# Performance work log

Measured on AMD Instinct MI355X. Metric: run time of the kernel, lower is better.

Reference implementation:

```python
import jax, jax.numpy as jnp
import numpy as np

EMBED_DIM = 128
FFN_DIM = 512
N_NODES = 50000
N_EDGES = 800000
LN_EPS = 1e-5


def setup_inputs() -> dict:
    key = jax.random.key(0)
    ks = jax.random.split(key, 8)
    s = 1.0 / np.sqrt(EMBED_DIM)
    return {
        "x": jax.random.normal(ks[0], (N_NODES, EMBED_DIM), jnp.float32),
        "edge_indices": jax.random.randint(ks[1], (2, N_EDGES), 0, N_NODES, dtype=jnp.int32),
        "W_qkv": jax.random.normal(ks[2], (EMBED_DIM, 3 * EMBED_DIM), jnp.float32) * s,
        "b_qkv": jnp.zeros((3 * EMBED_DIM,), jnp.float32),
        "W1": jax.random.normal(ks[3], (EMBED_DIM, FFN_DIM), jnp.float32) * s,
        "b1": jnp.zeros((FFN_DIM,), jnp.float32),
        "W2": jax.random.normal(ks[4], (FFN_DIM, EMBED_DIM), jnp.float32) * (1.0 / np.sqrt(FFN_DIM)),
        "b2": jnp.zeros((EMBED_DIM,), jnp.float32),
        "g1": jnp.ones((EMBED_DIM,), jnp.float32),
        "be1": jnp.zeros((EMBED_DIM,), jnp.float32),
        "g2": jnp.ones((EMBED_DIM,), jnp.float32),
        "be2": jnp.zeros((EMBED_DIM,), jnp.float32),
    }


def _layernorm(x, g, b):
    mu = jnp.mean(x, axis=-1, keepdims=True)
    var = jnp.mean(jnp.square(x - mu), axis=-1, keepdims=True)
    return (x - mu) * jax.lax.rsqrt(var + LN_EPS) * g + b


def _self_attention(x, edge_indices, W_qkv, b_qkv):
    n = x.shape[0]
    scale = x.shape[1] ** (-0.5)
    qkv = x @ W_qkv + b_qkv
    q, k, v = jnp.split(qkv, 3, axis=1)
    src, dst = edge_indices[0], edge_indices[1]  # row (softmax segment), col
    # per-edge logits: [E]
    alpha = jnp.sum(q[src] * k[dst], axis=1) * scale
    # segment (per-row) stable softmax
    m = jax.ops.segment_max(alpha, src, num_segments=n)
    e = jnp.exp(alpha - m[src])
    denom = jax.ops.segment_sum(e, src, num_segments=n)
    w = e / denom[src]  # [E]
    # sparse.mm: out[i] = sum_{(i,j) in E} w_ij * v[j]
    return jax.ops.segment_sum(w[:, None] * v[dst], src, num_segments=n)


def reference(x, edge_indices, W_qkv, b_qkv, W1, b1, W2, b2, g1, be1, g2, be2):
    # norm_first = False (post-norm), dropout = 0
    x = _layernorm(x + _self_attention(x, edge_indices, W_qkv, b_qkv), g1, be1)
    h = jax.nn.relu(x @ W1 + b1) @ W2 + b2
    x = _layernorm(x + h, g2, be2)
    return x
```

## Files before the change

### kernel.cpp

```cpp
#include <hip/hip_runtime.h>
#include <math.h>

#define NN 50000
#define NE 800000
#define ED 128
#define FD 512
#define QKV_BLOCKS (NN / 16)
#define HIST_BLOCKS ((NE / 4 + 255) / 256)
#define SCAN_BLOCKS ((NN + 255) / 256)

typedef __attribute__((ext_vector_type(8))) short bf16x8;
typedef __attribute__((ext_vector_type(4))) float f32x4;

static __device__ __forceinline__ float wave_sum(float x) {
#pragma unroll
  for (int off = 32; off > 0; off >>= 1) x += __shfl_xor(x, off, 64);
  return x;
}

static __device__ __forceinline__ int wave_sum_i(int x) {
#pragma unroll
  for (int off = 32; off > 0; off >>= 1) x += __shfl_xor(x, off, 64);
  return x;
}

static __device__ __forceinline__ unsigned short f2bf(float f) {
  union { float f; unsigned u; } c; c.f = f;
  unsigned r = c.u + 0x7fffu + ((c.u >> 16) & 1u);
  return (unsigned short)(r >> 16);
}

static __device__ __forceinline__ float2 bfpair(unsigned u) {
  union { unsigned a; float f; } lo, hi;
  lo.a = u << 16; hi.a = u & 0xffff0000u;
  return make_float2(lo.f, hi.f);
}

__global__ void k_prep(const float* __restrict__ Wqkv, const float* __restrict__ W1,
                       const float* __restrict__ W2, unsigned short* __restrict__ WqkvF,
                       unsigned short* __restrict__ W1F, unsigned short* __restrict__ W2F,
                       int* __restrict__ deg) {
  int idx = blockIdx.x * 256 + threadIdx.x;
  if (idx < NN) deg[idx] = 0;
  if (idx < 49152) {
    int j = idx & 7, l = (idx >> 3) & 63, kb = (idx >> 9) & 3, t = idx >> 11;
    int k = kb * 32 + (l >> 4) * 8 + j, n = t * 16 + (l & 15);
    WqkvF[idx] = f2bf(Wqkv[k * 384 + n]);
  }
  {
    int j = idx & 7, l = (idx >> 3) & 63, kb = (idx >> 9) & 3, t = idx >> 11;
    int k = kb * 32 + (l >> 4) * 8 + j, n = t * 16 + (l & 15);
    W1F[idx] = f2bf(W1[k * 512 + n]);
  }
  {
    int j = idx & 7, l = (idx >> 3) & 63, kb = (idx >> 9) & 15, t = idx >> 13;
    int k = kb * 32 + (l >> 4) * 8 + j, n = t * 16 + (l & 15);
    W2F[idx] = f2bf(W2[k * 128 + n]);
  }
}

__global__ __launch_bounds__(256) void k_qkv_hist(
    const float* __restrict__ X, const unsigned short* __restrict__ WqkvF,
    const float* __restrict__ B, unsigned short* __restrict__ q,
    unsigned short* __restrict__ k, unsigned short* __restrict__ v,
    const int* __restrict__ src, int* __restrict__ deg) {
  __shared__ unsigned short xs[16][136];
  const int tid = threadIdx.x;
  if (blockIdx.x >= QKV_BLOCKS) {
    const int e0 = ((blockIdx.x - QKV_BLOCKS) * 256 + tid) * 4;
    if (e0 < NE) {
      int4 s4 = *(const int4*)&src[e0];
      atomicAdd(&deg[s4.x], 1);
      atomicAdd(&deg[s4.y], 1);
      atomicAdd(&deg[s4.z], 1);
      atomicAdd(&deg[s4.w], 1);
    }
    return;
  }
  const int row0 = blockIdx.x * 16;
  for (int idx = tid; idx < 512; idx += 256) {
    int r = idx >> 5, c4 = (idx & 31) << 2;
    float4 val = *(const float4*)&X[(size_t)(row0 + r) * ED + c4];
    xs[r][c4] = f2bf(val.x); xs[r][c4 + 1] = f2bf(val.y);
    xs[r][c4 + 2] = f2bf(val.z); xs[r][c4 + 3] = f2bf(val.w);
  }
  __syncthreads();
  const int wv = tid >> 6, lane = tid & 63;
  const int ln = lane & 15, quad = lane >> 4;
  const int koff = quad * 8;
  bf16x8 a[4];
#pragma unroll
  for (int kb = 0; kb < 4; kb++) a[kb] = *(const bf16x8*)&xs[ln][kb * 32 + koff];
  for (int g = 0; g < 3; g++) {
    const int t0 = wv * 6 + g * 2;
    bf16x8 b[2][4];
#pragma unroll
    for (int j = 0; j < 2; j++)
#pragma unroll
      for (int kb = 0; kb < 4; kb++)
        b[j][kb] = *(const bf16x8*)&WqkvF[(size_t)(((t0 + j) * 4 + kb) * 64 + lane) * 8];
    f32x4 acc[2];
#pragma unroll
    for (int j = 0; j < 2; j++) acc[j] = (f32x4){0.f, 0.f, 0.f, 0.f};
#pragma unroll
    for (int kb = 0; kb < 4; kb++)
#pragma unroll
      for (int j = 0; j < 2; j++)
        acc[j] = __builtin_amdgcn_mfma_f32_16x16x32_bf16(a[kb], b[j][kb], acc[j], 0, 0, 0);
#pragma unroll
    for (int j = 0; j < 2; j++) {
      const int col = (t0 + j) * 16 + ln;
      const float bias = B[col];
      unsigned short* dst = (col < 128) ? q : (col < 256) ? k : v;
      const int c = col & 127;
#pragma unroll
      for (int r = 0; r < 4; r++)
        dst[(size_t)(row0 + quad * 4 + r) * ED + c] = f2bf(acc[j][r] + bias);
    }
  }
}

__global__ __launch_bounds__(256) void k_scan1(const int* __restrict__ deg,
                                               int* __restrict__ blocksum) {
  const int tid = threadIdx.x;
  const int i = blockIdx.x * 256 + tid;
  int d = (i < NN) ? deg[i] : 0;
  int w = wave_sum_i(d);
  __shared__ int ws[4];
  if ((tid & 63) == 0) ws[tid >> 6] = w;
  __syncthreads();
  if (tid == 0) blocksum[blockIdx.x] = ws[0] + ws[1] + ws[2] + ws[3];
}

__global__ __launch_bounds__(256) void k_scan3(const int* __restrict__ deg,
                                               const int* __restrict__ blocksum,
                                               int* __restrict__ row_start,
                                               int* __restrict__ cursor) {
  __shared__ int bs[256];
  __shared__ int s[256];
  const int t = threadIdx.x;
  int bsv = (t < SCAN_BLOCKS) ? blocksum[t] : 0;
  bs[t] = bsv;
  __syncthreads();
  for (int off = 1; off < 256; off <<= 1) {
    int add = (t >= off) ? bs[t - off] : 0;
    __syncthreads();
    bs[t] += add;
    __syncthreads();
  }
  const int blockpre = (blockIdx.x > 0) ? bs[blockIdx.x - 1] : 0;
  const int i = blockIdx.x * 256 + t;
  int d = (i < NN) ? deg[i] : 0;
  s[t] = d;
  __syncthreads();
  for (int off = 1; off < 256; off <<= 1) {
    int add = (t >= off) ? s[t - off] : 0;
    __syncthreads();
    s[t] += add;
    __syncthreads();
  }
  const int pre = blockpre + s[t] - d;
  if (i < NN) {
    row_start[i] = pre;
    cursor[i] = pre;
  }
  if (i == NN) row_start[NN] = pre;
}

__global__ void k_scatter(const int* __restrict__ src, const int* __restrict__ dst,
                          int* __restrict__ cursor, int* __restrict__ colidx) {
  const int e0 = (blockIdx.x * 256 + threadIdx.x) * 4;
  if (e0 < NE) {
    int4 s4 = *(const int4*)&src[e0];
    int4 d4 = *(const int4*)&dst[e0];
    colidx[atomicAdd(&cursor[s4.x], 1)] = d4.x;
    colidx[atomicAdd(&cursor[s4.y], 1)] = d4.y;
    colidx[atomicAdd(&cursor[s4.z], 1)] = d4.z;
    colidx[atomicAdd(&cursor[s4.w], 1)] = d4.w;
  }
}

template <bool FULL>
static __device__ __forceinline__ void attn_chunk(
    int base, int cnt, int grp, int gl, int lane, const float* qf,
    const unsigned short* __restrict__ k, const unsigned short* __restrict__ v,
    const int* __restrict__ colidx, float& l, float* ax) {
  const int C = FULL ? 16 : cnt;
  int colreg = 0;
  if (lane < C) colreg = colidx[base + lane];
#pragma unroll
  for (int it = 0; it < 4; it++) {
    const int t = it * 4 + grp;
    const bool act = FULL || t < C;
    const int srcl = act ? t : 0;
    const int c = __shfl(colreg, srcl, 64);
    uint4 kw = *(const uint4*)&k[(size_t)c * ED + gl * 8];
    uint4 vw = *(const uint4*)&v[(size_t)c * ED + gl * 8];
    float2 k0 = bfpair(kw.x), k1 = bfpair(kw.y), k2 = bfpair(kw.z), k3 = bfpair(kw.w);
    float dot = qf[0] * k0.x + qf[1] * k0.y + qf[2] * k1.x + qf[3] * k1.y +
                qf[4] * k2.x + qf[5] * k2.y + qf[6] * k3.x + qf[7] * k3.y;
    dot += __shfl_xor(dot, 1, 64);
    dot += __shfl_xor(dot, 2, 64);
    dot += __shfl_xor(dot, 4, 64);
    dot += __shfl_xor(dot, 8, 64);
    const float e = act ? __expf(dot * 0.08838834764831845f) : 0.f;
    l += e;
    float2 v0 = bfpair(vw.x), v1 = bfpair(vw.y), v2 = bfpair(vw.z), v3 = bfpair(vw.w);
    ax[0] = fmaf(e, v0.x, ax[0]); ax[1] = fmaf(e, v0.y, ax[1]);
    ax[2] = fmaf(e, v1.x, ax[2]); ax[3] = fmaf(e, v1.y, ax[3]);
    ax[4] = fmaf(e, v2.x, ax[4]); ax[5] = fmaf(e, v2.y, ax[5]);
    ax[6] = fmaf(e, v3.x, ax[6]); ax[7] = fmaf(e, v3.y, ax[7]);
  }
}

__global__ __launch_bounds__(256) void k_attn_ln1(
    const unsigned short* __restrict__ q, const unsigned short* __restrict__ k,
    const unsigned short* __restrict__ v, const float* __restrict__ x,
    const int* __restrict__ row_start, const int* __restrict__ colidx,
    const float* __restrict__ g1, const float* __restrict__ be1,
    float* __restrict__ out) {
  const int wv = threadIdx.x >> 6;
  const int lane = threadIdx.x & 63;
  const int grp = lane >> 4, gl = lane & 15;
  const int node = blockIdx.x * 4 + wv;

  float qf[8];
  {
    uint4 qw = *(const uint4*)&q[(size_t)node * ED + gl * 8];
    float2 p0 = bfpair(qw.x), p1 = bfpair(qw.y), p2 = bfpair(qw.z), p3 = bfpair(qw.w);
    qf[0] = p0.x; qf[1] = p0.y; qf[2] = p1.x; qf[3] = p1.y;
    qf[4] = p2.x; qf[5] = p2.y; qf[6] = p3.x; qf[7] = p3.y;
  }
  const int r0 = row_start[node], r1 = row_start[node + 1];
  float l = 0.f;
  float ax[8] = {0.f, 0.f, 0.f, 0.f, 0.f, 0.f, 0.f, 0.f};
  int base = r0;
  for (; base + 16 <= r1; base += 16)
    attn_chunk<true>(base, 16, grp, gl, lane, qf, k, v, colidx, l, ax);
  if (base < r1)
    attn_chunk<false>(base, r1 - base, grp, gl, lane, qf, k, v, colidx, l, ax);

#pragma unroll
  for (int j = 0; j < 8; j++) {
    ax[j] += __shfl_xor(ax[j], 16, 64);
    ax[j] += __shfl_xor(ax[j], 32, 64);
  }
  l += __shfl_xor(l, 16, 64);
  l += __shfl_xor(l, 32, 64);

  const float inv = (r1 > r0) ? 1.0f / l : 0.f;
  const int d0 = gl * 8 + grp * 2;
  float sx = (grp == 0) ? ax[0] : (grp == 1) ? ax[2] : (grp == 2) ? ax[4] : ax[6];
  float sy = (grp == 0) ? ax[1] : (grp == 1) ? ax[3] : (grp == 2) ? ax[5] : ax[7];
  float2 xv = *(const float2*)&x[(size_t)node * ED + d0];
  float vx = xv.x + sx * inv;
  float vy = xv.y + sy * inv;
  float mean = wave_sum(vx + vy) * (1.f / ED);
  float dx = vx - mean, dy = vy - mean;
  float var = wave_sum(dx * dx + dy * dy) * (1.f / ED);
  float rstd = rsqrtf(var + 1e-5f);
  float2 gg = *(const float2*)&g1[d0];
  float2 bb = *(const float2*)&be1[d0];
  float2 o = make_float2(dx * rstd * gg.x + bb.x, dy * rstd * gg.y + bb.y);
  *(float2*)&out[(size_t)node * ED + d0] = o;
}

__global__ __launch_bounds__(256) void k_ffn_ln2(
    const float* __restrict__ x1, const unsigned short* __restrict__ W1F,
    const float* __restrict__ b1, const unsigned short* __restrict__ W2F,
    const float* __restrict__ b2, const float* __restrict__ g2,
    const float* __restrict__ be2, float* __restrict__ out) {
  __shared__ unsigned short xs[16][136];
  __shared__ unsigned short hs[16][520];
  float* ys = (float*)&hs[0][0];
  const int row0 = blockIdx.x * 16;
  const int tid = threadIdx.x;
  for (int idx = tid; idx < 512; idx += 256) {
    int r = idx >> 5, c4 = (idx & 31) << 2;
    float4 val = *(const float4*)&x1[(size_t)(row0 + r) * ED + c4];
    xs[r][c4] = f2bf(val.x); xs[r][c4 + 1] = f2bf(val.y);
    xs[r][c4 + 2] = f2bf(val.z); xs[r][c4 + 3] = f2bf(val.w);
  }
  __syncthreads();
  const int wv = tid >> 6, lane = tid & 63;
  const int ln = lane & 15, quad = lane >> 4;
  const int koff = quad * 8;
  bf16x8 a1[4];
#pragma unroll
  for (int kb = 0; kb < 4; kb++) a1[kb] = *(const bf16x8*)&xs[ln][kb * 32 + koff];
  for (int g = 0; g < 4; g++) {
    const int t0 = wv * 8 + g * 2;
    bf16x8 b[2][4];
#pragma unroll
    for (int j = 0; j < 2; j++)
#pragma unroll
      for (int kb = 0; kb < 4; kb++)
        b[j][kb] = *(const bf16x8*)&W1F[(size_t)(((t0 + j) * 4 + kb) * 64 + lane) * 8];
    f32x4 acc[2];
#pragma unroll
    for (int j = 0; j < 2; j++) acc[j] = (f32x4){0.f, 0.f, 0.f, 0.f};
#pragma unroll
    for (int kb = 0; kb < 4; kb++)
#pragma unroll
      for (int j = 0; j < 2; j++)
        acc[j] = __builtin_amdgcn_mfma_f32_16x16x32_bf16(a1[kb], b[j][kb], acc[j], 0, 0, 0);
#pragma unroll
    for (int j = 0; j < 2; j++) {
      const int col = (t0 + j) * 16 + ln;
      const float bias = b1[col];
#pragma unroll
      for (int r = 0; r < 4; r++)
        hs[quad * 4 + r][col] = f2bf(fmaxf(acc[j][r] + bias, 0.f));
    }
  }
  __syncthreads();
  f32x4 acc2[2];
  acc2[0] = (f32x4){0.f, 0.f, 0.f, 0.f};
  acc2[1] = (f32x4){0.f, 0.f, 0.f, 0.f};
  const int nt0 = wv * 2;
  for (int kg = 0; kg < 4; kg++) {
    bf16x8 a[4];
#pragma unroll
    for (int kk = 0; kk < 4; kk++)
      a[kk] = *(const bf16x8*)&hs[ln][(kg * 4 + kk) * 32 + koff];
    bf16x8 b[2][4];
#pragma unroll
    for (int nt = 0; nt < 2; nt++)
#pragma unroll
      for (int kk = 0; kk < 4; kk++)
        b[nt][kk] = *(const bf16x8*)&W2F[(size_t)(((nt0 + nt) * 16 + kg * 4 + kk) * 64 + lane) * 8];
#pragma unroll
    for (int kk = 0; kk < 4; kk++)
#pragma unroll
      for (int nt = 0; nt < 2; nt++)
        acc2[nt] = __builtin_amdgcn_mfma_f32_16x16x32_bf16(a[kk], b[nt][kk], acc2[nt], 0, 0, 0);
  }
  __syncthreads();
#pragma unroll
  for (int nt = 0; nt < 2; nt++) {
    const int col = (nt0 + nt) * 16 + ln;
    const float bias = b2[col];
#pragma unroll
    for (int r = 0; r < 4; r++)
      ys[(quad * 4 + r) * 132 + col] = acc2[nt][r] + bias;
  }
  __syncthreads();
  float2 gg = *(const float2*)&g2[2 * lane];
  float2 bbe = *(const float2*)&be2[2 * lane];
#pragma unroll
  for (int rr = 0; rr < 4; rr++) {
    const int r = wv * 4 + rr;
    const int row = row0 + r;
    float2 xr = *(const float2*)&out[(size_t)row * ED + 2 * lane];
    float vx = ys[r * 132 + 2 * lane] + xr.x;
    float vy = ys[r * 132 + 2 * lane + 1] + xr.y;
    float mean = wave_sum(vx + vy) * (1.f / ED);
    float dx = vx - mean, dy = vy - mean;
    float var = wave_sum(dx * dx + dy * dy) * (1.f / ED);
    float rstd = rsqrtf(var + 1e-5f);
    float2 o = make_float2(dx * rstd * gg.x + bbe.x, dy * rstd * gg.y + bbe.y);
    *(float2*)&out[(size_t)row * ED + 2 * lane] = o;
  }
}

extern "C" void kernel_launch(void* const* d_in, const int* in_sizes, int n_in,
                              void* d_out, int out_size, void* d_ws, size_t ws_size,
                              hipStream_t stream) {
  const float* x = (const float*)d_in[0];
  const int* ei = (const int*)d_in[1];
  const float* W_qkv = (const float*)d_in[2];
  const float* b_qkv = (const float*)d_in[3];
  const float* W1 = (const float*)d_in[4];
  const float* b1 = (const float*)d_in[5];
  const float* W2 = (const float*)d_in[6];
  const float* b2 = (const float*)d_in[7];
  const float* g1 = (const float*)d_in[8];
  const float* be1 = (const float*)d_in[9];
  const float* g2 = (const float*)d_in[10];
  const float* be2 = (const float*)d_in[11];
  float* out = (float*)d_out;

  char* ws = (char*)d_ws;
  size_t off = 0;
  auto alloc = [&](size_t bytes) -> char* {
    char* p = ws + off;
    off = (off + bytes + 255) & ~(size_t)255;
    return p;
  };
  unsigned short* q = (unsigned short*)alloc(2 * (size_t)NN * ED);
  unsigned short* k = (unsigned short*)alloc(2 * (size_t)NN * ED);
  unsigned short* v = (unsigned short*)alloc(2 * (size_t)NN * ED);
  unsigned short* WqkvF = (unsigned short*)alloc(2 * 24 * 4 * 64 * 8);
  unsigned short* W1F = (unsigned short*)alloc(2 * 32 * 4 * 64 * 8);
  unsigned short* W2F = (unsigned short*)alloc(2 * 8 * 16 * 64 * 8);
  int* deg = (int*)alloc(sizeof(int) * NN);
  int* cursor = (int*)alloc(sizeof(int) * NN);
  int* row_start = (int*)alloc(sizeof(int) * (NN + 1));
  int* colidx = (int*)alloc(sizeof(int) * NE);
  int* blocksum = (int*)alloc(sizeof(int) * SCAN_BLOCKS);

  k_prep<<<256, 256, 0, stream>>>(W_qkv, W1, W2, WqkvF, W1F, W2F, deg);
  k_qkv_hist<<<QKV_BLOCKS + HIST_BLOCKS, 256, 0, stream>>>(x, WqkvF, b_qkv, q, k, v, ei, deg);
  k_scan1<<<SCAN_BLOCKS, 256, 0, stream>>>(deg, blocksum);
  k_scan3<<<SCAN_BLOCKS, 256, 0, stream>>>(deg, blocksum, row_start, cursor);
  k_scatter<<<HIST_BLOCKS, 256, 0, stream>>>(ei, ei + NE, cursor, colidx);
  k_attn_ln1<<<NN / 4, 256, 0, stream>>>(q, k, v, x, row_start, colidx, g1, be1, out);
  k_ffn_ln2<<<NN / 16, 256, 0, stream>>>(out, W1F, b1, W2F, b2, g2, be2, out);
}
```

Measured before the change: 293.6 us.

## Interleave K/V rows, prescale Q, and process two nodes per wave in attention

K and V are stored interleaved in one 256-wide row per node, so each gathered neighbour's key and value sit in adjacent memory. The softmax scale is folded into Q when it is written, removing a multiply per edge. Each wave now handles two nodes at once, issuing independent gathers for both so more loads are in flight and fewer waves are needed. The cost is higher register pressure and more control-flow variants when the two nodes have different degrees.

New measurement: 345.0 us. 17.5% more time.

```diff
diff --git a/kernel.cpp b/kernel.cpp
--- a/kernel.cpp
+++ b/kernel.cpp
@@ -62,8 +62,8 @@
 __global__ __launch_bounds__(256) void k_qkv_hist(
     const float* __restrict__ X, const unsigned short* __restrict__ WqkvF,
     const float* __restrict__ B, unsigned short* __restrict__ q,
-    unsigned short* __restrict__ k, unsigned short* __restrict__ v,
-    const int* __restrict__ src, int* __restrict__ deg) {
+    unsigned short* __restrict__ kv, const int* __restrict__ src,
+    int* __restrict__ deg) {
   __shared__ unsigned short xs[16][136];
   const int tid = threadIdx.x;
   if (blockIdx.x >= QKV_BLOCKS) {
@@ -111,11 +111,16 @@
     for (int j = 0; j < 2; j++) {
       const int col = (t0 + j) * 16 + ln;
       const float bias = B[col];
-      unsigned short* dst = (col < 128) ? q : (col < 256) ? k : v;
-      const int c = col & 127;
-#pragma unroll
-      for (int r = 0; r < 4; r++)
-        dst[(size_t)(row0 + quad * 4 + r) * ED + c] = f2bf(acc[j][r] + bias);
+      if (col < 128) {
+#pragma unroll
+        for (int r = 0; r < 4; r++)
+          q[(size_t)(row0 + quad * 4 + r) * ED + col] =
+              f2bf((acc[j][r] + bias) * 0.08838834764831845f);
+      } else {
+#pragma unroll
+        for (int r = 0; r < 4; r++)
+          kv[(size_t)(row0 + quad * 4 + r) * 256 + (col - 128)] = f2bf(acc[j][r] + bias);
+      }
     }
   }
 }
@@ -180,75 +185,76 @@
   }
 }
 
-template <bool FULL>
-static __device__ __forceinline__ void attn_chunk(
-    int base, int cnt, int grp, int gl, int lane, const float* qf,
-    const unsigned short* __restrict__ k, const unsigned short* __restrict__ v,
-    const int* __restrict__ colidx, float& l, float* ax) {
-  const int C = FULL ? 16 : cnt;
-  int colreg = 0;
-  if (lane < C) colreg = colidx[base + lane];
+template <bool DA, bool DB, bool FULL>
+static __device__ __forceinline__ void attn2(
+    int baseA, int cA, int baseB, int cB, int grp, int gl, int lane,
+    const float* qa, const float* qb, const unsigned short* __restrict__ kv,
+    const int* __restrict__ colidx, float& lA, float& lB, float* axA, float* axB) {
+  int col = 0;
+  const int idx = lane & 15;
+  if (DA && lane < 16) {
+    if (FULL || idx < cA) col = colidx[baseA + idx];
+  }
+  if (DB && lane >= 16 && lane < 32) {
+    if (FULL || idx < cB) col = colidx[baseB + idx];
+  }
 #pragma unroll
   for (int it = 0; it < 4; it++) {
     const int t = it * 4 + grp;
-    const bool act = FULL || t < C;
-    const int srcl = act ? t : 0;
-    const int c = __shfl(colreg, srcl, 64);
-    uint4 kw = *(const uint4*)&k[(size_t)c * ED + gl * 8];
-    uint4 vw = *(const uint4*)&v[(size_t)c * ED + gl * 8];
-    float2 k0 = bfpair(kw.x), k1 = bfpair(kw.y), k2 = bfpair(kw.z), k3 = bfpair(kw.w);
-    float dot = qf[0] * k0.x + qf[1] * k0.y + qf[2] * k1.x + qf[3] * k1.y +
-                qf[4] * k2.x + qf[5] * k2.y + qf[6] * k3.x + qf[7] * k3.y;
-    dot += __shfl_xor(dot, 1, 64);
-    dot += __shfl_xor(dot, 2, 64);
-    dot += __shfl_xor(dot, 4, 64);
-    dot += __shfl_xor(dot, 8, 64);
-    const float e = act ? __expf(dot * 0.08838834764831845f) : 0.f;
-    l += e;
-    float2 v0 = bfpair(vw.x), v1 = bfpair(vw.y), v2 = bfpair(vw.z), v3 = bfpair(vw.w);
-    ax[0] = fmaf(e, v0.x, ax[0]); ax[1] = fmaf(e, v0.y, ax[1]);
-    ax[2] = fmaf(e, v1.x, ax[2]); ax[3] = fmaf(e, v1.y, ax[3]);
-    ax[4] = fmaf(e, v2.x, ax[4]); ax[5] = fmaf(e, v2.y, ax[5]);
-    ax[6] = fmaf(e, v3.x, ax[6]); ax[7] = fmaf(e, v3.y, ax[7]);
-  }
-}
-
-__global__ __launch_bounds__(256) void k_attn_ln1(
-    const unsigned short* __restrict__ q, const unsigned short* __restrict__ k,
-    const unsigned short* __restrict__ v, const float* __restrict__ x,
-    const int* __restrict__ row_start, const int* __restrict__ colidx,
-    const float* __restrict__ g1, const float* __restrict__ be1,
-    float* __restrict__ out) {
-  const int wv = threadIdx.x >> 6;
-  const int lane = threadIdx.x & 63;
-  const int grp = lane >> 4, gl = lane & 15;
-  const int node = blockIdx.x * 4 + wv;
-
-  float qf[8];
-  {
-    uint4 qw = *(const uint4*)&q[(size_t)node * ED + gl * 8];
-    float2 p0 = bfpair(qw.x), p1 = bfpair(qw.y), p2 = bfpair(qw.z), p3 = bfpair(qw.w);
-    qf[0] = p0.x; qf[1] = p0.y; qf[2] = p1.x; qf[3] = p1.y;
-    qf[4] = p2.x; qf[5] = p2.y; qf[6] = p3.x; qf[7] = p3.y;
-  }
-  const int r0 = row_start[node], r1 = row_start[node + 1];
-  float l = 0.f;
-  float ax[8] = {0.f, 0.f, 0.f, 0.f, 0.f, 0.f, 0.f, 0.f};
-  int base = r0;
-  for (; base + 16 <= r1; base += 16)
-    attn_chunk<true>(base, 16, grp, gl, lane, qf, k, v, colidx, l, ax);
-  if (base < r1)
-    attn_chunk<false>(base, r1 - base, grp, gl, lane, qf, k, v, colidx, l, ax);
-
-#pragma unroll
-  for (int j = 0; j < 8; j++) {
-    ax[j] += __shfl_xor(ax[j], 16, 64);
-    ax[j] += __shfl_xor(ax[j], 32, 64);
-  }
-  l += __shfl_xor(l, 16, 64);
-  l += __shfl_xor(l, 32, 64);
-
-  const float inv = (r1 > r0) ? 1.0f / l : 0.f;
+    uint4 kwA, vwA, kwB, vwB;
+    bool actA = false, actB = false;
+    if (DA) {
+      actA = FULL || t < cA;
+      const int cc = __shfl(col, actA ? t : 0, 64);
+      kwA = *(const uint4*)&kv[(size_t)cc * 256 + gl * 8];
+      vwA = *(const uint4*)&kv[(size_t)cc * 256 + 128 + gl * 8];
+    }
+    if (DB) {
+      actB = FULL || t < cB;
+      const int cc = __shfl(col, 16 + (actB ? t : 0), 64);
+      kwB = *(const uint4*)&kv[(size_t)cc * 256 + gl * 8];
+      vwB = *(const uint4*)&kv[(size_t)cc * 256 + 128 + gl * 8];
+    }
+    if (DA) {
+      float2 k0 = bfpair(kwA.x), k1 = bfpair(kwA.y), k2 = bfpair(kwA.z), k3 = bfpair(kwA.w);
+      float dot = qa[0] * k0.x + qa[1] * k0.y + qa[2] * k1.x + qa[3] * k1.y +
+                  qa[4] * k2.x + qa[5] * k2.y + qa[6] * k3.x + qa[7] * k3.y;
+      dot += __shfl_xor(dot, 1, 64);
+      dot += __shfl_xor(dot, 2, 64);
+      dot += __shfl_xor(dot, 4, 64);
+      dot += __shfl_xor(dot, 8, 64);
+      const float e = actA ? __expf(dot) : 0.f;
+      lA += e;
+      float2 v0 = bfpair(vwA.x), v1 = bfpair(vwA.y), v2 = bfpair(vwA.z), v3 = bfpair(vwA.w);
+      axA[0] = fmaf(e, v0.x, axA[0]); axA[1] = fmaf(e, v0.y, axA[1]);
+      axA[2] = fmaf(e, v1.x, axA[2]); axA[3] = fmaf(e, v1.y, axA[3]);
+      axA[4] = fmaf(e, v2.x, axA[4]); axA[5] = fmaf(e, v2.y, axA[5]);
+      axA[6] = fmaf(e, v3.x, axA[6]); axA[7] = fmaf(e, v3.y, axA[7]);
+    }
+    if (DB) {
+      float2 k0 = bfpair(kwB.x), k1 = bfpair(kwB.y), k2 = bfpair(kwB.z), k3 = bfpair(kwB.w);
+      float dot = qb[0] * k0.x + qb[1] * k0.y + qb[2] * k1.x + qb[3] * k1.y +
+                  qb[4] * k2.x + qb[5] * k2.y + qb[6] * k3.x + qb[7] * k3.y;
+      dot += __shfl_xor(dot, 1, 64);
+      dot += __shfl_xor(dot, 2, 64);
+      dot += __shfl_xor(dot, 4, 64);
+      dot += __shfl_xor(dot, 8, 64);
+      const float e = actB ? __expf(dot) : 0.f;
+      lB += e;
+      float2 v0 = bfpair(vwB.x), v1 = bfpair(vwB.y), v2 = bfpair(vwB.z), v3 = bfpair(vwB.w);
+      axB[0] = fmaf(e, v0.x, axB[0]); axB[1] = fmaf(e, v0.y, axB[1]);
+      axB[2] = fmaf(e, v1.x, axB[2]); axB[3] = fmaf(e, v1.y, axB[3]);
+      axB[4] = fmaf(e, v2.x, axB[4]); axB[5] = fmaf(e, v2.y, axB[5]);
+      axB[6] = fmaf(e, v3.x, axB[6]); axB[7] = fmaf(e, v3.y, axB[7]);
+    }
+  }
+}
+
+static __device__ __forceinline__ void ln_store(
+    int node, int grp, int gl, float l, int cnt, const float* ax,
+    const float* __restrict__ x, const float* __restrict__ g1,
+    const float* __restrict__ be1, float* __restrict__ out) {
+  const float inv = (cnt > 0) ? 1.0f / l : 0.f;
   const int d0 = gl * 8 + grp * 2;
   float sx = (grp == 0) ? ax[0] : (grp == 1) ? ax[2] : (grp == 2) ? ax[4] : ax[6];
   float sy = (grp == 0) ? ax[1] : (grp == 1) ? ax[3] : (grp == 2) ? ax[5] : ax[7];
@@ -261,8 +267,83 @@
   float rstd = rsqrtf(var + 1e-5f);
   float2 gg = *(const float2*)&g1[d0];
   float2 bb = *(const float2*)&be1[d0];
-  float2 o = make_float2(dx * rstd * gg.x + bb.x, dy * rstd * gg.y + bb.y);
-  *(float2*)&out[(size_t)node * ED + d0] = o;
+  *(float2*)&out[(size_t)node * ED + d0] =
+      make_float2(dx * rstd * gg.x + bb.x, dy * rstd * gg.y + bb.y);
+}
+
+__global__ __launch_bounds__(256) void k_attn_ln1(
+    const unsigned short* __restrict__ q, const unsigned short* __restrict__ kv,
+    const float* __restrict__ x, const int* __restrict__ row_start,
+    const int* __restrict__ colidx, const float* __restrict__ g1,
+    const float* __restrict__ be1, float* __restrict__ out) {
+  const int wv = threadIdx.x >> 6;
+  const int lane = threadIdx.x & 63;
+  const int grp = lane >> 4, gl = lane & 15;
+  const int nodeA = blockIdx.x * 8 + wv * 2;
+
+  float qa[8], qb[8];
+  {
+    uint4 qw = *(const uint4*)&q[(size_t)nodeA * ED + gl * 8];
+    float2 p0 = bfpair(qw.x), p1 = bfpair(qw.y), p2 = bfpair(qw.z), p3 = bfpair(qw.w);
+    qa[0] = p0.x; qa[1] = p0.y; qa[2] = p1.x; qa[3] = p1.y;
+    qa[4] = p2.x; qa[5] = p2.y; qa[6] = p3.x; qa[7] = p3.y;
+  }
+  {
+    uint4 qw = *(const uint4*)&q[(size_t)(nodeA + 1) * ED + gl * 8];
+    float2 p0 = bfpair(qw.x), p1 = bfpair(qw.y), p2 = bfpair(qw.z), p3 = bfpair(qw.w);
+    qb[0] = p0.x; qb[1] = p0.y; qb[2] = p1.x; qb[3] = p1.y;
+    qb[4] = p2.x; qb[5] = p2.y; qb[6] = p3.x; qb[7] = p3.y;
+  }
+  const int rA0 = row_start[nodeA];
+  const int rA1 = row_start[nodeA + 1];
+  const int rB1 = row_start[nodeA + 2];
+  int baseA = rA0, baseB = rA1;
+  float lA = 0.f, lB = 0.f;
+  float axA[8] = {0.f, 0.f, 0.f, 0.f, 0.f, 0.f, 0.f, 0.f};
+  float axB[8] = {0.f, 0.f, 0.f, 0.f, 0.f, 0.f, 0.f, 0.f};
+
+  const int fA = (rA1 - rA0) >> 4, fB = (rB1 - rA1) >> 4;
+  const int both = fA < fB ? fA : fB;
+  for (int i = 0; i < both; i++) {
+    attn2<true, true, true>(baseA, 16, baseB, 16, grp, gl, lane, qa, qb, kv,
+                            colidx, lA, lB, axA, axB);
+    baseA += 16; baseB += 16;
+  }
+  for (int i = both; i < fA; i++) {
+    attn2<true, false, true>(baseA, 16, 0, 0, grp, gl, lane, qa, qb, kv,
+                             colidx, lA, lB, axA, axB);
+    baseA += 16;
+  }
+  for (int i = both; i < fB; i++) {
+    attn2<false, true, true>(0, 0, baseB, 16, grp, gl, lane, qa, qb, kv,
+                             colidx, lA, lB, axA, axB);
+    baseB += 16;
+  }
+  const int tA = rA1 - baseA, tB = rB1 - baseB;
+  if (tA && tB)
+    attn2<true, true, false>(baseA, tA, baseB, tB, grp, gl, lane, qa, qb, kv,
+                             colidx, lA, lB, axA, axB);
+  else if (tA)
+    attn2<true, false, false>(baseA, tA, 0, 0, grp, gl, lane, qa, qb, kv,
+                              colidx, lA, lB, axA, axB);
+  else if (tB)
+    attn2<false, true, false>(0, 0, baseB, tB, grp, gl, lane, qa, qb, kv,
+                              colidx, lA, lB, axA, axB);
+
+#pragma unroll
+  for (int j = 0; j < 8; j++) {
+    axA[j] += __shfl_xor(axA[j], 16, 64);
+    axA[j] += __shfl_xor(axA[j], 32, 64);
+    axB[j] += __shfl_xor(axB[j], 16, 64);
+    axB[j] += __shfl_xor(axB[j], 32, 64);
+  }
+  lA += __shfl_xor(lA, 16, 64);
+  lA += __shfl_xor(lA, 32, 64);
+  lB += __shfl_xor(lB, 16, 64);
+  lB += __shfl_xor(lB, 32, 64);
+
+  ln_store(nodeA, grp, gl, lA, rA1 - rA0, axA, x, g1, be1, out);
+  ln_store(nodeA + 1, grp, gl, lB, rB1 - rA1, axB, x, g1, be1, out);
 }
 
 __global__ __launch_bounds__(256) void k_ffn_ln2(
@@ -388,8 +469,7 @@
     return p;
   };
   unsigned short* q = (unsigned short*)alloc(2 * (size_t)NN * ED);
-  unsigned short* k = (unsigned short*)alloc(2 * (size_t)NN * ED);
-  unsigned short* v = (unsigned short*)alloc(2 * (size_t)NN * ED);
+  unsigned short* kv = (unsigned short*)alloc(2 * (size_t)NN * 256);
   unsigned short* WqkvF = (unsigned short*)alloc(2 * 24 * 4 * 64 * 8);
   unsigned short* W1F = (unsigned short*)alloc(2 * 32 * 4 * 64 * 8);
   unsigned short* W2F = (unsigned short*)alloc(2 * 8 * 16 * 64 * 8);
@@ -400,10 +480,10 @@
   int* blocksum = (int*)alloc(sizeof(int) * SCAN_BLOCKS);
 
   k_prep<<<256, 256, 0, stream>>>(W_qkv, W1, W2, WqkvF, W1F, W2F, deg);
-  k_qkv_hist<<<QKV_BLOCKS + HIST_BLOCKS, 256, 0, stream>>>(x, WqkvF, b_qkv, q, k, v, ei, deg);
+  k_qkv_hist<<<QKV_BLOCKS + HIST_BLOCKS, 256, 0, stream>>>(x, WqkvF, b_qkv, q, kv, ei, deg);
   k_scan1<<<SCAN_BLOCKS, 256, 0, stream>>>(deg, blocksum);
   k_scan3<<<SCAN_BLOCKS, 256, 0, stream>>>(deg, blocksum, row_start, cursor);
   k_scatter<<<HIST_BLOCKS, 256, 0, stream>>>(ei, ei + NE, cursor, colidx);
-  k_attn_ln1<<<NN / 4, 256, 0, stream>>>(q, k, v, x, row_start, colidx, g1, be1, out);
+  k_attn_ln1<<<NN / 8, 256, 0, stream>>>(q, kv, x, row_start, colidx, g1, be1, out);
   k_ffn_ln2<<<NN / 16, 256, 0, stream>>>(out, W1F, b1, W2F, b2, g2, be2, out);
 }
```

## Interleave K/V rows, store QKV in fp16, use fdot2 and packed half accumulation

Applied to the files above, without the earlier changes.

Stores K and V interleaved per node in one 256-wide fp16 buffer, so each edge's gathered K and V share a row and locality. Switches Q/K/V from bf16 to fp16, folds the softmax scale into Q, uses fdot2 for the logit and packed half2 FMA for the value accumulation. The tail chunk loop now only iterates over the active groups. Accumulating in fp16 is cheaper in ALU work and registers but risks precision loss or overflow, since the exp weights are not max-subtracted.

Result: no change. 295.0 us (+0.5%).

```diff
diff --git a/kernel.cpp b/kernel.cpp
--- a/kernel.cpp
+++ b/kernel.cpp
@@ -11,6 +11,7 @@
 
 typedef __attribute__((ext_vector_type(8))) short bf16x8;
 typedef __attribute__((ext_vector_type(4))) float f32x4;
+typedef _Float16 half2_t __attribute__((ext_vector_type(2)));
 
 static __device__ __forceinline__ float wave_sum(float x) {
 #pragma unroll
@@ -30,11 +31,23 @@
   return (unsigned short)(r >> 16);
 }
 
-static __device__ __forceinline__ float2 bfpair(unsigned u) {
-  union { unsigned a; float f; } lo, hi;
-  lo.a = u << 16; hi.a = u & 0xffff0000u;
-  return make_float2(lo.f, hi.f);
-}
+static __device__ __forceinline__ unsigned short f2h(float f) {
+  union { _Float16 h; unsigned short u; } c; c.h = (_Float16)f;
+  return c.u;
+}
+
+static __device__ __forceinline__ half2_t u2h2(unsigned u) {
+  union { unsigned u; half2_t h; } c; c.u = u;
+  return c.h;
+}
+
+#if __has_builtin(__builtin_amdgcn_fdot2)
+#define FDOT2(a, b, c) __builtin_amdgcn_fdot2((a), (b), (c), false)
+#else
+static __device__ __forceinline__ float FDOT2(half2_t a, half2_t b, float c) {
+  return (float)a[0] * (float)b[0] + (float)a[1] * (float)b[1] + c;
+}
+#endif
 
 __global__ void k_prep(const float* __restrict__ Wqkv, const float* __restrict__ W1,
                        const float* __restrict__ W2, unsigned short* __restrict__ WqkvF,
@@ -62,8 +75,8 @@
 __global__ __launch_bounds__(256) void k_qkv_hist(
     const float* __restrict__ X, const unsigned short* __restrict__ WqkvF,
     const float* __restrict__ B, unsigned short* __restrict__ q,
-    unsigned short* __restrict__ k, unsigned short* __restrict__ v,
-    const int* __restrict__ src, int* __restrict__ deg) {
+    unsigned short* __restrict__ kv, const int* __restrict__ src,
+    int* __restrict__ deg) {
   __shared__ unsigned short xs[16][136];
   const int tid = threadIdx.x;
   if (blockIdx.x >= QKV_BLOCKS) {
@@ -111,11 +124,16 @@
     for (int j = 0; j < 2; j++) {
       const int col = (t0 + j) * 16 + ln;
       const float bias = B[col];
-      unsigned short* dst = (col < 128) ? q : (col < 256) ? k : v;
-      const int c = col & 127;
-#pragma unroll
-      for (int r = 0; r < 4; r++)
-        dst[(size_t)(row0 + quad * 4 + r) * ED + c] = f2bf(acc[j][r] + bias);
+      if (col < 128) {
+#pragma unroll
+        for (int r = 0; r < 4; r++)
+          q[(size_t)(row0 + quad * 4 + r) * ED + col] =
+              f2h((acc[j][r] + bias) * 0.08838834764831845f);
+      } else {
+#pragma unroll
+        for (int r = 0; r < 4; r++)
+          kv[(size_t)(row0 + quad * 4 + r) * 256 + (col - 128)] = f2h(acc[j][r] + bias);
+      }
     }
   }
 }
@@ -182,76 +200,78 @@
 
 template <bool FULL>
 static __device__ __forceinline__ void attn_chunk(
-    int base, int cnt, int grp, int gl, int lane, const float* qf,
-    const unsigned short* __restrict__ k, const unsigned short* __restrict__ v,
-    const int* __restrict__ colidx, float& l, float* ax) {
+    int base, int cnt, int grp, int gl, int lane, const half2_t* qh,
+    const unsigned short* __restrict__ kv, const int* __restrict__ colidx,
+    float& l, half2_t* axh) {
   const int C = FULL ? 16 : cnt;
   int colreg = 0;
   if (lane < C) colreg = colidx[base + lane];
-#pragma unroll
-  for (int it = 0; it < 4; it++) {
+  const int itmax = FULL ? 4 : ((C + 3) >> 2);
+#pragma unroll(FULL ? 4 : 1)
+  for (int it = 0; it < itmax; it++) {
     const int t = it * 4 + grp;
     const bool act = FULL || t < C;
-    const int srcl = act ? t : 0;
-    const int c = __shfl(colreg, srcl, 64);
-    uint4 kw = *(const uint4*)&k[(size_t)c * ED + gl * 8];
-    uint4 vw = *(const uint4*)&v[(size_t)c * ED + gl * 8];
-    float2 k0 = bfpair(kw.x), k1 = bfpair(kw.y), k2 = bfpair(kw.z), k3 = bfpair(kw.w);
-    float dot = qf[0] * k0.x + qf[1] * k0.y + qf[2] * k1.x + qf[3] * k1.y +
-                qf[4] * k2.x + qf[5] * k2.y + qf[6] * k3.x + qf[7] * k3.y;
+    const int cc = __shfl(colreg, act ? t : 0, 64);
+    const unsigned short* row = &kv[(size_t)cc * 256 + gl * 8];
+    uint4 kw = *(const uint4*)row;
+    uint4 vw = *(const uint4*)(row + 128);
+    float dot = FDOT2(qh[0], u2h2(kw.x), 0.f);
+    dot = FDOT2(qh[1], u2h2(kw.y), dot);
+    dot = FDOT2(qh[2], u2h2(kw.z), dot);
+    dot = FDOT2(qh[3], u2h2(kw.w), dot);
     dot += __shfl_xor(dot, 1, 64);
     dot += __shfl_xor(dot, 2, 64);
     dot += __shfl_xor(dot, 4, 64);
     dot += __shfl_xor(dot, 8, 64);
-    const float e = act ? __expf(dot * 0.08838834764831845f) : 0.f;
+    const float e = act ? __expf(dot) : 0.f;
     l += e;
-    float2 v0 = bfpair(vw.x), v1 = bfpair(vw.y), v2 = bfpair(vw.z), v3 = bfpair(vw.w);
-    ax[0] = fmaf(e, v0.x, ax[0]); ax[1] = fmaf(e, v0.y, ax[1]);
-    ax[2] = fmaf(e, v1.x, ax[2]); ax[3] = fmaf(e, v1.y, ax[3]);
-    ax[4] = fmaf(e, v2.x, ax[4]); ax[5] = fmaf(e, v2.y, ax[5]);
-    ax[6] = fmaf(e, v3.x, ax[6]); ax[7] = fmaf(e, v3.y, ax[7]);
+    const half2_t e2 = {(_Float16)e, (_Float16)e};
+    axh[0] += e2 * u2h2(vw.x);
+    axh[1] += e2 * u2h2(vw.y);
+    axh[2] += e2 * u2h2(vw.z);
+    axh[3] += e2 * u2h2(vw.w);
   }
 }
 
 __global__ __launch_bounds__(256) void k_attn_ln1(
-    const unsigned short* __restrict__ q, const unsigned short* __restrict__ k,
-    const unsigned short* __restrict__ v, const float* __restrict__ x,
-    const int* __restrict__ row_start, const int* __restrict__ colidx,
-    const float* __restrict__ g1, const float* __restrict__ be1,
-    float* __restrict__ out) {
+    const unsigned short* __restrict__ q, const unsigned short* __restrict__ kv,
+    const float* __restrict__ x, const int* __restrict__ row_start,
+    const int* __restrict__ colidx, const float* __restrict__ g1,
+    const float* __restrict__ be1, float* __restrict__ out) {
   const int wv = threadIdx.x >> 6;
   const int lane = threadIdx.x & 63;
   const int grp = lane >> 4, gl = lane & 15;
   const int node = blockIdx.x * 4 + wv;
 
-  float qf[8];
+  half2_t qh[4];
   {
     uint4 qw = *(const uint4*)&q[(size_t)node * ED + gl * 8];
-    float2 p0 = bfpair(qw.x), p1 = bfpair(qw.y), p2 = bfpair(qw.z), p3 = bfpair(qw.w);
-    qf[0] = p0.x; qf[1] = p0.y; qf[2] = p1.x; qf[3] = p1.y;
-    qf[4] = p2.x; qf[5] = p2.y; qf[6] = p3.x; qf[7] = p3.y;
+    qh[0] = u2h2(qw.x); qh[1] = u2h2(qw.y);
+    qh[2] = u2h2(qw.z); qh[3] = u2h2(qw.w);
   }
   const int r0 = row_start[node], r1 = row_start[node + 1];
   float l = 0.f;
-  float ax[8] = {0.f, 0.f, 0.f, 0.f, 0.f, 0.f, 0.f, 0.f};
+  half2_t axh[4] = {};
   int base = r0;
   for (; base + 16 <= r1; base += 16)
-    attn_chunk<true>(base, 16, grp, gl, lane, qf, k, v, colidx, l, ax);
+    attn_chunk<true>(base, 16, grp, gl, lane, qh, kv, colidx, l, axh);
   if (base < r1)
-    attn_chunk<false>(base, r1 - base, grp, gl, lane, qf, k, v, colidx, l, ax);
-
-#pragma unroll
-  for (int j = 0; j < 8; j++) {
-    ax[j] += __shfl_xor(ax[j], 16, 64);
-    ax[j] += __shfl_xor(ax[j], 32, 64);
+    attn_chunk<false>(base, r1 - base, grp, gl, lane, qh, kv, colidx, l, axh);
+
+#pragma unroll
+  for (int j = 0; j < 4; j++) {
+    union { half2_t h; int i; } c;
+    union { int i; half2_t h; } d;
+    c.h = axh[j]; d.i = __shfl_xor(c.i, 16, 64); axh[j] += d.h;
+    c.h = axh[j]; d.i = __shfl_xor(c.i, 32, 64); axh[j] += d.h;
   }
   l += __shfl_xor(l, 16, 64);
   l += __shfl_xor(l, 32, 64);
 
   const float inv = (r1 > r0) ? 1.0f / l : 0.f;
   const int d0 = gl * 8 + grp * 2;
-  float sx = (grp == 0) ? ax[0] : (grp == 1) ? ax[2] : (grp == 2) ? ax[4] : ax[6];
-  float sy = (grp == 0) ? ax[1] : (grp == 1) ? ax[3] : (grp == 2) ? ax[5] : ax[7];
+  const half2_t s = (grp == 0) ? axh[0] : (grp == 1) ? axh[1] : (grp == 2) ? axh[2] : axh[3];
+  const float sx = (float)s[0], sy = (float)s[1];
   float2 xv = *(const float2*)&x[(size_t)node * ED + d0];
   float vx = xv.x + sx * inv;
   float vy = xv.y + sy * inv;
@@ -388,8 +408,7 @@
     return p;
   };
   unsigned short* q = (unsigned short*)alloc(2 * (size_t)NN * ED);
-  unsigned short* k = (unsigned short*)alloc(2 * (size_t)NN * ED);
-  unsigned short* v = (unsigned short*)alloc(2 * (size_t)NN * ED);
+  unsigned short* kv = (unsigned short*)alloc(2 * (size_t)NN * 256);
   unsigned short* WqkvF = (unsigned short*)alloc(2 * 24 * 4 * 64 * 8);
   unsigned short* W1F = (unsigned short*)alloc(2 * 32 * 4 * 64 * 8);
   unsigned short* W2F = (unsigned short*)alloc(2 * 8 * 16 * 64 * 8);
@@ -400,10 +419,10 @@
   int* blocksum = (int*)alloc(sizeof(int) * SCAN_BLOCKS);
 
   k_prep<<<256, 256, 0, stream>>>(W_qkv, W1, W2, WqkvF, W1F, W2F, deg);
-  k_qkv_hist<<<QKV_BLOCKS + HIST_BLOCKS, 256, 0, stream>>>(x, WqkvF, b_qkv, q, k, v, ei, deg);
+  k_qkv_hist<<<QKV_BLOCKS + HIST_BLOCKS, 256, 0, stream>>>(x, WqkvF, b_qkv, q, kv, ei, deg);
   k_scan1<<<SCAN_BLOCKS, 256, 0, stream>>>(deg, blocksum);
   k_scan3<<<SCAN_BLOCKS, 256, 0, stream>>>(deg, blocksum, row_start, cursor);
   k_scatter<<<HIST_BLOCKS, 256, 0, stream>>>(ei, ei + NE, cursor, colidx);
-  k_attn_ln1<<<NN / 4, 256, 0, stream>>>(q, k, v, x, row_start, colidx, g1, be1, out);
+  k_attn_ln1<<<NN / 4, 256, 0, stream>>>(q, kv, x, row_start, colidx, g1, be1, out);
   k_ffn_ln2<<<NN / 16, 256, 0, stream>>>(out, W1F, b1, W2F, b2, g2, be2, out);
 }
```
